# Performance work log

Measured on AMD Instinct MI355X. Metric: run time of the kernel, lower is better.

## Reference

```python
import jax, jax.numpy as jnp
import numpy as np

N = 100_000          # nodes
E = 1_600_000        # directed edges
GENE_DIM = 39
NUM_CLASSES = 5
EPS = 1e-5           # BatchNorm1d eps
DIMS = [(GENE_DIM, 64), (64, 128), (128, 64), (64, 32)]


def setup_inputs() -> dict:
    key = jax.random.key(0)
    ks = jax.random.split(key, 32)
    inp = {
        "x": jax.random.normal(ks[0], (N, GENE_DIM), dtype=jnp.float32),
        "edge_index": jax.random.randint(ks[1], (2, E), 0, N, dtype=jnp.int64),
    }
    ki = 2
    for i, (din, dout) in enumerate(DIMS, start=1):
        scale = 1.0 / np.sqrt(din)
        inp[f"W{i}"] = jax.random.uniform(ks[ki], (din, dout), jnp.float32, -scale, scale); ki += 1
        inp[f"b{i}"] = jnp.zeros((dout,), jnp.float32)
        inp[f"g{i}"] = jnp.ones((dout,), jnp.float32)    # BN gamma
        inp[f"be{i}"] = jnp.zeros((dout,), jnp.float32)  # BN beta
    scale = 1.0 / np.sqrt(32)
    inp["Wc"] = jax.random.uniform(ks[ki], (32, NUM_CLASSES), jnp.float32, -scale, scale)
    inp["bc"] = jnp.zeros((NUM_CLASSES,), jnp.float32)
    return inp


def reference(x, edge_index,
              W1, b1, g1, be1,
              W2, b2, g2, be2,
              W3, b3, g3, be3,
              W4, b4, g4, be4,
              Wc, bc):
    n = x.shape[0]
    # --- self loops + symmetric GCN normalization (shared by all 4 convs) ---
    loop = jnp.arange(n, dtype=edge_index.dtype)
    src = jnp.concatenate([edge_index[0], loop])   # message source (x_j)
    dst = jnp.concatenate([edge_index[1], loop])   # aggregation target
    deg = jax.ops.segment_sum(jnp.ones_like(dst, dtype=x.dtype), dst, num_segments=n)
    dinv = jnp.where(deg > 0, jax.lax.rsqrt(deg), 0.0)
    norm = (dinv[src] * dinv[dst])[:, None]        # [E+n, 1]

    def conv(h, W, b):
        # linear transform, gather from source, normalize, scatter-add at target
        m = (h @ W)[src] * norm
        return jax.ops.segment_sum(m, dst, num_segments=n) + b

    def bn(h, g, be):
        # training-mode BatchNorm1d: biased variance over the node axis
        mu = jnp.mean(h, axis=0)
        var = jnp.mean(jnp.square(h - mu), axis=0)
        return g * (h - mu) * jax.lax.rsqrt(var + EPS) + be

    h = bn(jax.nn.relu(conv(x, W1, b1)), g1, be1)
    h = bn(jax.nn.relu(conv(h, W2, b2)), g2, be2)
    h = bn(jax.nn.relu(conv(h, W3, b3)), g3, be3)
    h = bn(jax.nn.relu(conv(h, W4, b4)), g4, be4)
    out = h @ Wc + bc
    return (out, h)
```

## Files before the change

kernel.cpp:

```cpp
#include <hip/hip_runtime.h>

typedef unsigned int uint;
typedef unsigned short ushort;
typedef __attribute__((ext_vector_type(8))) short bf16x8;
typedef __attribute__((ext_vector_type(4))) float f32x4;

#define N_NODES 100000
#define N_EDGES 1600000
#define NB_C 256
#define TILE_C ((N_EDGES + NB_C - 1) / NB_C)
#define NB_D ((N_NODES + 511) / 512)
#define MG_GRID ((N_NODES + 63) / 64)
#define AGG_GRID 2048
constexpr float BN_EPS = 1e-5f;

__device__ __forceinline__ float bflo(uint w) { return __uint_as_float(w << 16); }
__device__ __forceinline__ float bfhi(uint w) { return __uint_as_float(w & 0xffff0000u); }
__device__ __forceinline__ ushort f2bf(float x) {
    uint u = __float_as_uint(x);
    uint r = (u + 0x7fffu + ((u >> 16) & 1u)) >> 16;
    return (ushort)r;
}
__device__ __forceinline__ uint pack2(float a, float b) {
    return (uint)f2bf(a) | ((uint)f2bf(b) << 16);
}

__global__ void detect_kernel(const int* __restrict__ ep, int* __restrict__ flag)
{
    __shared__ int cnt;
    if (threadIdx.x == 0) cnt = 0;
    __syncthreads();
    int nz = 0;
    for (int k = threadIdx.x; k < 1024; k += blockDim.x)
        if (ep[2 * k + 1] != 0) nz++;
    atomicAdd(&cnt, nz);
    __syncthreads();
    if (threadIdx.x == 0) *flag = (cnt == 0) ? 1 : 0;
}

__global__ __launch_bounds__(256) void coarseA_kernel(const int* __restrict__ ep,
                                                      const int* __restrict__ flag,
                                                      uint* __restrict__ ch)
{
    __shared__ uint lh[256];
    int t = threadIdx.x, blk = blockIdx.x;
    lh[t] = 0;
    __syncthreads();
    bool i64 = (*flag != 0);
    int start = blk * TILE_C;
    int end = start + TILE_C;
    if (end > N_EDGES) end = N_EDGES;
    for (int e = start + t; e < end; e += 256) {
        int d = i64 ? ep[2 * (N_EDGES + e)] : ep[N_EDGES + e];
        atomicAdd(&lh[d >> 9], 1u);
    }
    __syncthreads();
    ch[t * NB_C + blk] = lh[t];
}

__global__ void scanB_kernel(uint* __restrict__ ch, uint* __restrict__ bucketBase)
{
    __shared__ uint tot[256];
    int t = threadIdx.x;
    uint s = 0;
    for (int i = 0; i < NB_C; i++) s += ch[t * NB_C + i];
    tot[t] = s;
    __syncthreads();
    for (int off = 1; off < 256; off <<= 1) {
        uint add = (t >= off) ? tot[t - off] : 0u;
        __syncthreads();
        tot[t] += add;
        __syncthreads();
    }
    uint base = tot[t] - s;
    bucketBase[t] = base;
    if (t == 255) bucketBase[256] = base + s;
    uint run = base;
    for (int i = 0; i < NB_C; i++) {
        uint c = ch[t * NB_C + i];
        ch[t * NB_C + i] = run;
        run += c;
    }
}

__global__ __launch_bounds__(256) void scatterC_kernel(const int* __restrict__ ep,
                                                       const int* __restrict__ flag,
                                                       const uint* __restrict__ ch,
                                                       int2* __restrict__ pair)
{
    __shared__ uint loff[256];
    int t = threadIdx.x, blk = blockIdx.x;
    loff[t] = ch[t * NB_C + blk];
    __syncthreads();
    bool i64 = (*flag != 0);
    int start = blk * TILE_C;
    int end = start + TILE_C;
    if (end > N_EDGES) end = N_EDGES;
    for (int e = start + t; e < end; e += 256) {
        int s, d;
        if (i64) { s = ep[2 * e]; d = ep[2 * (N_EDGES + e)]; }
        else     { s = ep[e];     d = ep[N_EDGES + e]; }
        uint pos = atomicAdd(&loff[d >> 9], 1u);
        pair[pos] = make_int2(s, d);
    }
}

__global__ __launch_bounds__(256) void bucketD_kernel(const int2* __restrict__ pair,
                                                      const uint* __restrict__ bucketBase,
                                                      int* __restrict__ rowptr,
                                                      float* __restrict__ dinv,
                                                      int* __restrict__ colidx)
{
    __shared__ uint cnt[512], offp[512], s2[256];
    int bin = blockIdx.x, t = threadIdx.x;
    cnt[t] = 0; cnt[t + 256] = 0;
    __syncthreads();
    uint lo = bucketBase[bin], hi = bucketBase[bin + 1];
    for (uint p = lo + t; p < hi; p += 256)
        atomicAdd(&cnt[pair[p].y & 511], 1u);
    __syncthreads();
    uint a = cnt[2 * t], b = cnt[2 * t + 1];
    s2[t] = a + b;
    __syncthreads();
    for (int off = 1; off < 256; off <<= 1) {
        uint add = (t >= off) ? s2[t - off] : 0u;
        __syncthreads();
        s2[t] += add;
        __syncthreads();
    }
    uint excl = s2[t] - (a + b);
    offp[2 * t] = excl;
    offp[2 * t + 1] = excl + a;
    __syncthreads();
    for (int k = t; k < 512; k += 256) {
        int d = bin * 512 + k;
        if (d < N_NODES) {
            rowptr[d] = (int)(lo + offp[k]);
            dinv[d] = rsqrtf((float)(cnt[k] + 1));
        }
    }
    if (bin == 0 && t == 0) rowptr[N_NODES] = N_EDGES;
    __syncthreads();
    for (uint p = lo + t; p < hi; p += 256) {
        int2 pr = pair[p];
        uint pos = lo + atomicAdd(&offp[pr.y & 511], 1u);
        colidx[pos] = pr.x;
    }
}

__global__ __launch_bounds__(256) void xscale_kernel(const float* __restrict__ x,
                                                     const float* __restrict__ dinv,
                                                     ushort* __restrict__ xs)
{
    int idx = blockIdx.x * 256 + threadIdx.x;
    if (idx >= N_NODES * 40) return;
    int i = idx / 40;
    int c = idx - i * 40;
    float v = (c < 39) ? x[i * 39 + c] * dinv[i] : 0.f;
    xs[idx] = f2bf(v);
}

__global__ void packW_kernel(const float* __restrict__ W, ushort* __restrict__ out,
                             int din, int dout, int K)
{
    int CT = dout >> 4;
    int tot = (K >> 5) * CT * 64 * 8;
    for (int idx = blockIdx.x * 256 + threadIdx.x; idx < tot; idx += gridDim.x * 256) {
        int j = idx & 7;
        int lane = (idx >> 3) & 63;
        int slot = idx >> 9;
        int ct = slot % CT, kt = slot / CT;
        int k = kt * 32 + (lane >> 4) * 8 + j;
        int c = ct * 16 + (lane & 15);
        float v = (k < din) ? W[k * dout + c] : 0.f;
        out[idx] = f2bf(v);
    }
}

__global__ __launch_bounds__(256) void agg1_kernel(
    const uint* __restrict__ xs, const int* __restrict__ rowptr,
    const int* __restrict__ colidx, const float* __restrict__ dinv,
    uint* __restrict__ outU, float* __restrict__ rowsumP)
{
    int lane = threadIdx.x & 63, wid = threadIdx.x >> 6;
    int part = lane >> 5, idx = lane & 31;
    bool feat = idx < 20, dlane = (idx == 20);
    int gw = blockIdx.x * 4 + wid, nw = gridDim.x * 4;
    for (int i = gw; i < N_NODES; i += nw) {
        int iu = __builtin_amdgcn_readfirstlane(i);
        int s0 = rowptr[iu], e0 = rowptr[iu + 1];
        float ax = 0.f, ay = 0.f, ad = 0.f;
        if (!part && feat) { uint w = xs[iu * 20 + idx]; ax = bflo(w); ay = bfhi(w); }
        int e = s0 + part;
        for (; e + 6 < e0; e += 8) {
            int j0 = colidx[e], j1 = colidx[e + 2], j2 = colidx[e + 4], j3 = colidx[e + 6];
            if (feat) {
                uint w0 = xs[j0 * 20 + idx], w1 = xs[j1 * 20 + idx];
                uint w2 = xs[j2 * 20 + idx], w3 = xs[j3 * 20 + idx];
                ax += bflo(w0); ay += bfhi(w0);
                ax += bflo(w1); ay += bfhi(w1);
                ax += bflo(w2); ay += bfhi(w2);
                ax += bflo(w3); ay += bfhi(w3);
            } else if (dlane) {
                ad += dinv[j0] + dinv[j1] + dinv[j2] + dinv[j3];
            }
        }
        for (; e < e0; e += 2) {
            int j = colidx[e];
            if (feat) { uint w = xs[j * 20 + idx]; ax += bflo(w); ay += bfhi(w); }
            else if (dlane) ad += dinv[j];
        }
        ax += __shfl_xor(ax, 32);
        ay += __shfl_xor(ay, 32);
        ad += __shfl_xor(ad, 32);
        float di = dinv[iu];
        float dtot = __shfl(ad, 20);
        if (!part) outU[iu * 32 + idx] = feat ? pack2(di * ax, di * ay) : 0u;
        if (lane == 0) rowsumP[iu] = di * (dtot + di);
    }
}

__global__ __launch_bounds__(256) void agg_only64_kernel(
    const uint* __restrict__ zs, const int* __restrict__ rowptr,
    const int* __restrict__ colidx, const float* __restrict__ dinv,
    uint* __restrict__ out)
{
    int lane = threadIdx.x & 63, wid = threadIdx.x >> 6;
    int part = lane >> 5, fl = lane & 31;
    int gw = blockIdx.x * 4 + wid, nw = gridDim.x * 4;
    for (int i = gw; i < N_NODES; i += nw) {
        int iu = __builtin_amdgcn_readfirstlane(i);
        int s0 = rowptr[iu], e0 = rowptr[iu + 1];
        float ax = 0.f, ay = 0.f;
        if (!part) { uint w = zs[iu * 32 + fl]; ax = bflo(w); ay = bfhi(w); }
        int e = s0 + part;
        for (; e + 6 < e0; e += 8) {
            int j0 = colidx[e], j1 = colidx[e + 2], j2 = colidx[e + 4], j3 = colidx[e + 6];
            uint w0 = zs[j0 * 32 + fl], w1 = zs[j1 * 32 + fl];
            uint w2 = zs[j2 * 32 + fl], w3 = zs[j3 * 32 + fl];
            ax += bflo(w0); ay += bfhi(w0);
            ax += bflo(w1); ay += bfhi(w1);
            ax += bflo(w2); ay += bfhi(w2);
            ax += bflo(w3); ay += bfhi(w3);
        }
        for (; e < e0; e += 2) {
            uint w = zs[colidx[e] * 32 + fl];
            ax += bflo(w); ay += bfhi(w);
        }
        ax += __shfl_xor(ax, 32);
        ay += __shfl_xor(ay, 32);
        if (!part) {
            float di = dinv[iu];
            out[iu * 32 + fl] = pack2(di * ax, di * ay);
        }
    }
}

__global__ __launch_bounds__(256) void agg_relu64_kernel(
    const uint* __restrict__ zs, const int* __restrict__ rowptr,
    const int* __restrict__ colidx, const float* __restrict__ dinv,
    const float* __restrict__ bias, uint* __restrict__ outT,
    float* __restrict__ Psum, float* __restrict__ Psq)
{
    int lane = threadIdx.x & 63, wid = threadIdx.x >> 6;
    int part = lane >> 5, fl = lane & 31;
    int gw = blockIdx.x * 4 + wid, nw = gridDim.x * 4;
    float bx = bias[2 * fl], by = bias[2 * fl + 1];
    float lsx = 0.f, lsy = 0.f, lqx = 0.f, lqy = 0.f;
    for (int i = gw; i < N_NODES; i += nw) {
        int iu = __builtin_amdgcn_readfirstlane(i);
        int s0 = rowptr[iu], e0 = rowptr[iu + 1];
        float ax = 0.f, ay = 0.f;
        if (!part) { uint w = zs[iu * 32 + fl]; ax = bflo(w); ay = bfhi(w); }
        int e = s0 + part;
        for (; e + 6 < e0; e += 8) {
            int j0 = colidx[e], j1 = colidx[e + 2], j2 = colidx[e + 4], j3 = colidx[e + 6];
            uint w0 = zs[j0 * 32 + fl], w1 = zs[j1 * 32 + fl];
            uint w2 = zs[j2 * 32 + fl], w3 = zs[j3 * 32 + fl];
            ax += bflo(w0); ay += bfhi(w0);
            ax += bflo(w1); ay += bfhi(w1);
            ax += bflo(w2); ay += bfhi(w2);
            ax += bflo(w3); ay += bfhi(w3);
        }
        for (; e < e0; e += 2) {
            uint w = zs[colidx[e] * 32 + fl];
            ax += bflo(w); ay += bfhi(w);
        }
        ax += __shfl_xor(ax, 32);
        ay += __shfl_xor(ay, 32);
        if (!part) {
            float di = dinv[iu];
            float tx_ = fmaxf(fmaf(di, ax, bx), 0.f);
            float ty_ = fmaxf(fmaf(di, ay, by), 0.f);
            outT[iu * 32 + fl] = pack2(tx_, ty_);
            lsx += tx_; lsy += ty_;
            lqx += tx_ * tx_; lqy += ty_ * ty_;
        }
    }
    __shared__ float ssum[64], ssq[64];
    if (threadIdx.x < 64) { ssum[threadIdx.x] = 0.f; ssq[threadIdx.x] = 0.f; }
    __syncthreads();
    if (!part) {
        atomicAdd(&ssum[2 * fl], lsx); atomicAdd(&ssum[2 * fl + 1], lsy);
        atomicAdd(&ssq[2 * fl], lqx);  atomicAdd(&ssq[2 * fl + 1], lqy);
    }
    __syncthreads();
    if (threadIdx.x < 64) {
        Psum[threadIdx.x * gridDim.x + blockIdx.x] = ssum[threadIdx.x];
        Psq[threadIdx.x * gridDim.x + blockIdx.x] = ssq[threadIdx.x];
    }
}

__global__ __launch_bounds__(256) void agg_relu32_kernel(
    const uint* __restrict__ zs, const int* __restrict__ rowptr,
    const int* __restrict__ colidx, const float* __restrict__ dinv,
    const float* __restrict__ bias, float2* __restrict__ outT,
    float* __restrict__ Psum, float* __restrict__ Psq)
{
    int lane = threadIdx.x & 63, wid = threadIdx.x >> 6;
    int part = lane >> 4, fl = lane & 15;
    int gw = blockIdx.x * 4 + wid, nw = gridDim.x * 4;
    float bx = bias[2 * fl], by = bias[2 * fl + 1];
    float lsx = 0.f, lsy = 0.f, lqx = 0.f, lqy = 0.f;
    for (int i = gw; i < N_NODES; i += nw) {
        int iu = __builtin_amdgcn_readfirstlane(i);
        int s0 = rowptr[iu], e0 = rowptr[iu + 1];
        float ax = 0.f, ay = 0.f;
        if (part == 0) { uint w = zs[iu * 16 + fl]; ax = bflo(w); ay = bfhi(w); }
        int e = s0 + part;
        for (; e + 12 < e0; e += 16) {
            int j0 = colidx[e], j1 = colidx[e + 4], j2 = colidx[e + 8], j3 = colidx[e + 12];
            uint w0 = zs[j0 * 16 + fl], w1 = zs[j1 * 16 + fl];
            uint w2 = zs[j2 * 16 + fl], w3 = zs[j3 * 16 + fl];
            ax += bflo(w0); ay += bfhi(w0);
            ax += bflo(w1); ay += bfhi(w1);
            ax += bflo(w2); ay += bfhi(w2);
            ax += bflo(w3); ay += bfhi(w3);
        }
        for (; e < e0; e += 4) {
            uint w = zs[colidx[e] * 16 + fl];
            ax += bflo(w); ay += bfhi(w);
        }
        ax += __shfl_xor(ax, 16); ax += __shfl_xor(ax, 32);
        ay += __shfl_xor(ay, 16); ay += __shfl_xor(ay, 32);
        if (lane < 16) {
            float di = dinv[iu];
            float tx_ = fmaxf(fmaf(di, ax, bx), 0.f);
            float ty_ = fmaxf(fmaf(di, ay, by), 0.f);
            outT[iu * 16 + fl] = make_float2(tx_, ty_);
            lsx += tx_; lsy += ty_;
            lqx += tx_ * tx_; lqy += ty_ * ty_;
        }
    }
    __shared__ float ssum[32], ssq[32];
    if (threadIdx.x < 32) { ssum[threadIdx.x] = 0.f; ssq[threadIdx.x] = 0.f; }
    __syncthreads();
    if (lane < 16) {
        atomicAdd(&ssum[2 * fl], lsx); atomicAdd(&ssum[2 * fl + 1], lsy);
        atomicAdd(&ssq[2 * fl], lqx);  atomicAdd(&ssq[2 * fl + 1], lqy);
    }
    __syncthreads();
    if (threadIdx.x < 32) {
        Psum[threadIdx.x * gridDim.x + blockIdx.x] = ssum[threadIdx.x];
        Psq[threadIdx.x * gridDim.x + blockIdx.x] = ssq[threadIdx.x];
    }
}

template <int K, int DOUT, int MODE>
__global__ __launch_bounds__(256) void mgemm_kernel(
    const ushort* __restrict__ A, const ushort* __restrict__ Wfrag,
    const float* __restrict__ bias, const float* __restrict__ bias2,
    const float* __restrict__ rowsumP, const float* __restrict__ dinv,
    ushort* __restrict__ outB, float* __restrict__ Psum, float* __restrict__ Psq)
{
    constexpr int KT = K / 32, CT = DOUT / 16;
    int tid = threadIdx.x;
    int lane = tid & 63, wid = tid >> 6;
    int r0 = blockIdx.x * 64 + wid * 16;
    int arow = r0 + (lane & 15);
    if (arow >= N_NODES) arow = N_NODES - 1;
    const ushort* aptr = A + (size_t)arow * K + (lane >> 4) * 8;

    f32x4 acc[CT];
#pragma unroll
    for (int ct = 0; ct < CT; ct++) acc[ct] = (f32x4){0.f, 0.f, 0.f, 0.f};

#pragma unroll
    for (int kt = 0; kt < KT; kt++) {
        bf16x8 af = *(const bf16x8*)(aptr + kt * 32);
        const ushort* wp = Wfrag + ((size_t)(kt * CT) * 64 + lane) * 8;
#pragma unroll
        for (int ct = 0; ct < CT; ct++) {
            bf16x8 bfr = *(const bf16x8*)(wp + (size_t)ct * 64 * 8);
            acc[ct] = __builtin_amdgcn_mfma_f32_16x16x32_bf16(af, bfr, acc[ct], 0, 0, 0);
        }
    }

    int colbase = lane & 15;
    int rgrp = lane >> 4;
    int rows[4]; bool rok[4];
    float rP[4], rD[4];
#pragma unroll
    for (int i = 0; i < 4; i++) {
        int r = r0 + rgrp * 4 + i;
        rows[i] = r;
        rok[i] = (r < N_NODES);
        int rc = rok[i] ? r : 0;
        if constexpr (MODE == 1) rP[i] = rowsumP[rc];
        else rD[i] = dinv[rc];
    }

    __shared__ float ssum[DOUT], ssq[DOUT];
    if constexpr (MODE <= 1) {
        for (int c = tid; c < DOUT; c += 256) { ssum[c] = 0.f; ssq[c] = 0.f; }
        __syncthreads();
    }

#pragma unroll
    for (int ct = 0; ct < CT; ct++) {
        int col = ct * 16 + colbase;
        float b = bias[col];
        float b2 = 0.f;
        if constexpr (MODE == 1) b2 = bias2[col];
        float cs = 0.f, cq = 0.f;
#pragma unroll
        for (int i = 0; i < 4; i++) {
            float v = acc[ct][i] + b;
            if constexpr (MODE == 1) v = fmaf(rP[i], b2, v);
            if constexpr (MODE <= 1) v = fmaxf(v, 0.f);
            float w = (MODE == 1) ? v : rD[i] * v;
            if (rok[i]) {
                outB[(size_t)rows[i] * DOUT + col] = f2bf(w);
                if constexpr (MODE <= 1) { cs += v; cq += v * v; }
            }
        }
        if constexpr (MODE <= 1) {
            cs += __shfl_xor(cs, 16); cs += __shfl_xor(cs, 32);
            cq += __shfl_xor(cq, 16); cq += __shfl_xor(cq, 32);
            if (rgrp == 0) {
                atomicAdd(&ssum[col], cs);
                atomicAdd(&ssq[col], cq);
            }
        }
    }
    if constexpr (MODE <= 1) {
        __syncthreads();
        for (int c = tid; c < DOUT; c += 256) {
            Psum[(size_t)c * gridDim.x + blockIdx.x] = ssum[c];
            Psq[(size_t)c * gridDim.x + blockIdx.x] = ssq[c];
        }
    }
}

__global__ __launch_bounds__(256) void reduce_bn_kernel(
    const float* __restrict__ Psum, const float* __restrict__ Psq, int nb,
    const float* __restrict__ g, const float* __restrict__ be,
    float* __restrict__ sOut, float* __restrict__ uOut)
{
    int c = blockIdx.x, t = threadIdx.x;
    float s = 0.f, q = 0.f;
    for (int i = t; i < nb; i += 256) {
        s += Psum[(size_t)c * nb + i];
        q += Psq[(size_t)c * nb + i];
    }
    __shared__ float rs[256], rq[256];
    rs[t] = s; rq[t] = q;
    __syncthreads();
    for (int off = 128; off > 0; off >>= 1) {
        if (t < off) { rs[t] += rs[t + off]; rq[t] += rq[t + off]; }
        __syncthreads();
    }
    if (t == 0) {
        float mu = rs[0] * (1.0f / N_NODES);
        float var = rq[0] * (1.0f / N_NODES) - mu * mu;
        float sv = g[c] * rsqrtf(var + BN_EPS);
        sOut[c] = sv;
        uOut[c] = be[c] - mu * sv;
    }
}

__global__ void foldW_kernel(const float* __restrict__ W, const float* __restrict__ s,
                             const float* __restrict__ u, float* __restrict__ Wf,
                             float* __restrict__ v, int din, int dout)
{
    int c = blockIdx.x, t = threadIdx.x;
    float contrib = 0.f;
    if (t < din) {
        float w = W[t * dout + c];
        Wf[t * dout + c] = s[t] * w;
        contrib = u[t] * w;
    }
    __shared__ float red[128];
    red[t] = contrib;
    __syncthreads();
    for (int off = 64; off > 0; off >>= 1) {
        if (t < off) red[t] += red[t + off];
        __syncthreads();
    }
    if (t == 0) v[c] = red[0];
}

__global__ __launch_bounds__(256) void final_kernel(
    const float* __restrict__ t4, const float* __restrict__ sArr,
    const float* __restrict__ uArr, const float* __restrict__ Wc,
    const float* __restrict__ bc, float* __restrict__ out_logits,
    float* __restrict__ out_h)
{
    __shared__ float sc[32], sh2[32], Wcs[160], bcs[5];
    int t = threadIdx.x;
    if (t < 32) { sc[t] = sArr[t]; sh2[t] = uArr[t]; }
    if (t < 160) Wcs[t] = Wc[t];
    if (t < 5) bcs[t] = bc[t];
    __syncthreads();
    int i = blockIdx.x * blockDim.x + t;
    if (i >= N_NODES) return;
    float hv[32];
#pragma unroll
    for (int f0 = 0; f0 < 32; f0 += 4) {
        float4 v = *(const float4*)&t4[(size_t)i * 32 + f0];
        hv[f0 + 0] = fmaf(sc[f0 + 0], v.x, sh2[f0 + 0]);
        hv[f0 + 1] = fmaf(sc[f0 + 1], v.y, sh2[f0 + 1]);
        hv[f0 + 2] = fmaf(sc[f0 + 2], v.z, sh2[f0 + 2]);
        hv[f0 + 3] = fmaf(sc[f0 + 3], v.w, sh2[f0 + 3]);
    }
#pragma unroll
    for (int f0 = 0; f0 < 32; f0 += 4) {
        float4 v = {hv[f0], hv[f0 + 1], hv[f0 + 2], hv[f0 + 3]};
        *(float4*)&out_h[(size_t)i * 32 + f0] = v;
    }
    float o[5];
#pragma unroll
    for (int c = 0; c < 5; c++) o[c] = bcs[c];
#pragma unroll
    for (int f = 0; f < 32; f++) {
        float hvf = hv[f];
#pragma unroll
        for (int c = 0; c < 5; c++) o[c] = fmaf(hvf, Wcs[f * 5 + c], o[c]);
    }
#pragma unroll
    for (int c = 0; c < 5; c++) out_logits[(size_t)i * 5 + c] = o[c];
}

extern "C" void kernel_launch(void* const* d_in, const int* in_sizes, int n_in,
                              void* d_out, int out_size, void* d_ws, size_t ws_size,
                              hipStream_t stream)
{
    const float* x = (const float*)d_in[0];
    const int* ei = (const int*)d_in[1];
    const float* W1 = (const float*)d_in[2];
    const float* b1 = (const float*)d_in[3];
    const float* g1 = (const float*)d_in[4];
    const float* be1 = (const float*)d_in[5];
    const float* W2 = (const float*)d_in[6];
    const float* b2 = (const float*)d_in[7];
    const float* g2 = (const float*)d_in[8];
    const float* be2 = (const float*)d_in[9];
    const float* W3 = (const float*)d_in[10];
    const float* b3 = (const float*)d_in[11];
    const float* g3 = (const float*)d_in[12];
    const float* be3 = (const float*)d_in[13];
    const float* W4 = (const float*)d_in[14];
    const float* b4 = (const float*)d_in[15];
    const float* g4 = (const float*)d_in[16];
    const float* be4 = (const float*)d_in[17];
    const float* Wc = (const float*)d_in[18];
    const float* bc = (const float*)d_in[19];

    char* ws = (char*)d_ws;
    size_t off = 0;
    auto alloc = [&](size_t bytes) -> void* {
        void* p = ws + off;
        off += (bytes + 255) & ~(size_t)255;
        return p;
    };
    uint* ch = (uint*)alloc(65536 * 4);
    uint* bucketBase = (uint*)alloc(257 * 4);
    int2* pair = (int2*)alloc((size_t)N_EDGES * 8);
    int* rowptr = (int*)alloc((size_t)(N_NODES + 1) * 4);
    float* dinv = (float*)alloc((size_t)N_NODES * 4);
    int* colidx = (int*)alloc((size_t)N_EDGES * 4);
    int* flag = (int*)alloc(256);
    float* rowsumP = (float*)alloc((size_t)N_NODES * 4);
    ushort* xs = (ushort*)alloc((size_t)N_NODES * 40 * 2);
    float* Wf = (float*)alloc(128 * 128 * 4);
    ushort* Wfrag = (ushort*)alloc(32768);
    float* vB = (float*)alloc(128 * 4);
    float* sArr = (float*)alloc(128 * 4);
    float* uArr = (float*)alloc(128 * 4);
    float* Psum = (float*)alloc((size_t)128 * 2048 * 4);
    float* Psq = (float*)alloc((size_t)128 * 2048 * 4);
    uint* bufA = (uint*)alloc((size_t)N_NODES * 64 * 4);
    uint* bufB = (uint*)alloc((size_t)N_NODES * 32 * 4);
    uint* bufC = (uint*)alloc((size_t)N_NODES * 32 * 4);
    float* bufF = (float*)alloc((size_t)N_NODES * 32 * 4);
    if (off > ws_size) return;

    detect_kernel<<<1, 256, 0, stream>>>(ei, flag);
    coarseA_kernel<<<NB_C, 256, 0, stream>>>(ei, flag, ch);
    scanB_kernel<<<1, 256, 0, stream>>>(ch, bucketBase);
    scatterC_kernel<<<NB_C, 256, 0, stream>>>(ei, flag, ch, pair);
    bucketD_kernel<<<NB_D, 256, 0, stream>>>(pair, bucketBase, rowptr, dinv, colidx);

    xscale_kernel<<<(N_NODES * 40 + 255) / 256, 256, 0, stream>>>(x, dinv, xs);
    packW_kernel<<<16, 256, 0, stream>>>(W1, Wfrag, 39, 64, 64);

    agg1_kernel<<<AGG_GRID, 256, 0, stream>>>((const uint*)xs, rowptr, colidx, dinv,
                                              bufB, rowsumP);
    mgemm_kernel<64, 64, 0><<<MG_GRID, 256, 0, stream>>>(
        (const ushort*)bufB, Wfrag, b1, nullptr, nullptr, dinv,
        (ushort*)bufC, Psum, Psq);
    reduce_bn_kernel<<<64, 256, 0, stream>>>(Psum, Psq, MG_GRID, g1, be1, sArr, uArr);
    foldW_kernel<<<128, 128, 0, stream>>>(W2, sArr, uArr, Wf, vB, 64, 128);
    packW_kernel<<<32, 256, 0, stream>>>(Wf, Wfrag, 64, 128, 64);

    agg_only64_kernel<<<AGG_GRID, 256, 0, stream>>>(bufC, rowptr, colidx, dinv, bufB);
    mgemm_kernel<64, 128, 1><<<MG_GRID, 256, 0, stream>>>(
        (const ushort*)bufB, Wfrag, b2, vB, rowsumP, nullptr,
        (ushort*)bufA, Psum, Psq);
    reduce_bn_kernel<<<128, 256, 0, stream>>>(Psum, Psq, MG_GRID, g2, be2, sArr, uArr);
    foldW_kernel<<<64, 128, 0, stream>>>(W3, sArr, uArr, Wf, vB, 128, 64);
    packW_kernel<<<32, 256, 0, stream>>>(Wf, Wfrag, 128, 64, 128);

    mgemm_kernel<128, 64, 2><<<MG_GRID, 256, 0, stream>>>(
        (const ushort*)bufA, Wfrag, vB, nullptr, nullptr, dinv,
        (ushort*)bufB, nullptr, nullptr);
    agg_relu64_kernel<<<AGG_GRID, 256, 0, stream>>>(bufB, rowptr, colidx, dinv,
                                                    b3, bufC, Psum, Psq);
    reduce_bn_kernel<<<64, 256, 0, stream>>>(Psum, Psq, AGG_GRID, g3, be3, sArr, uArr);
    foldW_kernel<<<32, 128, 0, stream>>>(W4, sArr, uArr, Wf, vB, 64, 32);
    packW_kernel<<<16, 256, 0, stream>>>(Wf, Wfrag, 64, 32, 64);

    mgemm_kernel<64, 32, 2><<<MG_GRID, 256, 0, stream>>>(
        (const ushort*)bufC, Wfrag, vB, nullptr, nullptr, dinv,
        (ushort*)bufB, nullptr, nullptr);
    agg_relu32_kernel<<<AGG_GRID, 256, 0, stream>>>(bufB, rowptr, colidx, dinv,
                                                    b4, (float2*)bufF, Psum, Psq);
    reduce_bn_kernel<<<32, 256, 0, stream>>>(Psum, Psq, AGG_GRID, g4, be4, sArr, uArr);

    float* out_logits = (float*)d_out;
    float* out_h = (float*)d_out + (size_t)N_NODES * 5;
    final_kernel<<<(N_NODES + 255) / 256, 256, 0, stream>>>(bufF, sArr, uArr, Wc, bc,
                                                            out_logits, out_h);
}
```

Measured before the change: 382.4 us.

## Slice feature tables into 16-column planes and pin slices to XCDs in aggregation

Feature tables are stored as column slices of 16 bf16 values per node (32 bytes), and one templated aggregation kernel maps each slice to a subset of XCDs by block index. Each XCD's L2 then only has to hold one slice of the gathered table, which should raise cache hit rates for the random neighbor gathers. The GEMM kernels gain sliced input and output addressing, and the rowsum computation moves into its own kernel. The cost is an extra kernel, an extra memset for the padding slice, and 32-byte gathers that use less of each cache line per access.

```diff
diff --git a/kernel.cpp b/kernel.cpp
--- a/kernel.cpp
+++ b/kernel.cpp
@@ -11,7 +11,8 @@
 #define TILE_C ((N_EDGES + NB_C - 1) / NB_C)
 #define NB_D ((N_NODES + 511) / 512)
 #define MG_GRID ((N_NODES + 63) / 64)
-#define AGG_GRID 2048
+#define AGGS_GRID 1024
+#define AGGS_M (AGGS_GRID / 8)
 constexpr float BN_EPS = 1e-5f;
 
 __device__ __forceinline__ float bflo(uint w) { return __uint_as_float(w << 16); }
@@ -150,14 +151,18 @@
 
 __global__ __launch_bounds__(256) void xscale_kernel(const float* __restrict__ x,
                                                      const float* __restrict__ dinv,
-                                                     ushort* __restrict__ xs)
+                                                     uint* __restrict__ xs)
 {
     int idx = blockIdx.x * 256 + threadIdx.x;
-    if (idx >= N_NODES * 40) return;
-    int i = idx / 40;
-    int c = idx - i * 40;
-    float v = (c < 39) ? x[i * 39 + c] * dinv[i] : 0.f;
-    xs[idx] = f2bf(v);
+    if (idx >= N_NODES * 24) return;
+    int i = idx / 24;
+    int u = idx - i * 24;
+    int s = u >> 3, d = u & 7;
+    int c0 = 2 * u, c1 = 2 * u + 1;
+    float di = dinv[i];
+    float v0 = (c0 < 39) ? x[i * 39 + c0] * di : 0.f;
+    float v1 = (c1 < 39) ? x[i * 39 + c1] * di : 0.f;
+    xs[((size_t)s * N_NODES + i) * 8 + d] = pack2(v0, v1);
 }
 
 __global__ void packW_kernel(const float* __restrict__ W, ushort* __restrict__ out,
@@ -177,196 +182,123 @@
     }
 }
 
-__global__ __launch_bounds__(256) void agg1_kernel(
-    const uint* __restrict__ xs, const int* __restrict__ rowptr,
+__global__ __launch_bounds__(256) void rowsum_kernel(
+    const int* __restrict__ rowptr, const int* __restrict__ colidx,
+    const float* __restrict__ dinv, float* __restrict__ rowsumP)
+{
+    int tid = threadIdx.x;
+    int lane = tid & 63, wid = tid >> 6;
+    int g16 = lane >> 4, gl = lane & 15;
+    int gid = (blockIdx.x * 4 + wid) * 4 + g16;
+    int ng = gridDim.x * 16;
+    for (int i0 = gid; i0 < N_NODES; i0 += ng) {
+        int s0 = rowptr[i0], e0 = rowptr[i0 + 1];
+        float ad = 0.f;
+        for (int e = s0 + gl; e < e0; e += 16) ad += dinv[colidx[e]];
+        ad += __shfl_xor(ad, 1); ad += __shfl_xor(ad, 2);
+        ad += __shfl_xor(ad, 4); ad += __shfl_xor(ad, 8);
+        if (gl == 0) {
+            float di = dinv[i0];
+            rowsumP[i0] = di * (ad + di);
+        }
+    }
+}
+
+template <int SLICES, int MODE>
+__global__ __launch_bounds__(256) void aggs_kernel(
+    const uint* __restrict__ table, const int* __restrict__ rowptr,
     const int* __restrict__ colidx, const float* __restrict__ dinv,
-    uint* __restrict__ outU, float* __restrict__ rowsumP)
-{
-    int lane = threadIdx.x & 63, wid = threadIdx.x >> 6;
-    int part = lane >> 5, idx = lane & 31;
-    bool feat = idx < 20, dlane = (idx == 20);
-    int gw = blockIdx.x * 4 + wid, nw = gridDim.x * 4;
-    for (int i = gw; i < N_NODES; i += nw) {
-        int iu = __builtin_amdgcn_readfirstlane(i);
-        int s0 = rowptr[iu], e0 = rowptr[iu + 1];
-        float ax = 0.f, ay = 0.f, ad = 0.f;
-        if (!part && feat) { uint w = xs[iu * 20 + idx]; ax = bflo(w); ay = bfhi(w); }
-        int e = s0 + part;
+    const float* __restrict__ bias,
+    uint* __restrict__ outU, float* __restrict__ outF,
+    float* __restrict__ Psum, float* __restrict__ Psq)
+{
+    int bid = blockIdx.x;
+    int xcd = bid & 7;
+    int M = gridDim.x >> 3;
+    int slice, sub, ns;
+    if constexpr (SLICES == 4) { slice = xcd >> 1; sub = xcd & 1; ns = 2; }
+    else if constexpr (SLICES == 2) { slice = xcd >> 2; sub = xcd & 3; ns = 4; }
+    else {
+        if (xcd < 3) { slice = 0; sub = xcd; ns = 3; }
+        else if (xcd < 6) { slice = 1; sub = xcd - 3; ns = 3; }
+        else { slice = 2; sub = xcd - 6; ns = 2; }
+    }
+    int v = (bid >> 3) * ns + sub;
+    int V = M * ns;
+
+    int tid = threadIdx.x;
+    int lane = tid & 63, wid = tid >> 6;
+    int g16 = lane >> 4, gl = lane & 15;
+    int p = gl >> 3, d = gl & 7;
+    const uint* base = table + (size_t)slice * N_NODES * 8;
+
+    float bx = 0.f, by = 0.f;
+    if constexpr (MODE >= 1) {
+        bx = bias[slice * 16 + 2 * d];
+        by = bias[slice * 16 + 2 * d + 1];
+    }
+    float lsx = 0.f, lsy = 0.f, lqx = 0.f, lqy = 0.f;
+
+    for (int i0 = v * 16 + wid * 4 + g16; i0 < N_NODES; i0 += V * 16) {
+        int s0 = rowptr[i0], e0 = rowptr[i0 + 1];
+        float ax = 0.f, ay = 0.f;
+        if (p == 0) {
+            uint w = base[((size_t)i0 << 3) + d];
+            ax = bflo(w); ay = bfhi(w);
+        }
+        int e = s0 + p;
         for (; e + 6 < e0; e += 8) {
             int j0 = colidx[e], j1 = colidx[e + 2], j2 = colidx[e + 4], j3 = colidx[e + 6];
-            if (feat) {
-                uint w0 = xs[j0 * 20 + idx], w1 = xs[j1 * 20 + idx];
-                uint w2 = xs[j2 * 20 + idx], w3 = xs[j3 * 20 + idx];
-                ax += bflo(w0); ay += bfhi(w0);
-                ax += bflo(w1); ay += bfhi(w1);
-                ax += bflo(w2); ay += bfhi(w2);
-                ax += bflo(w3); ay += bfhi(w3);
-            } else if (dlane) {
-                ad += dinv[j0] + dinv[j1] + dinv[j2] + dinv[j3];
-            }
-        }
-        for (; e < e0; e += 2) {
-            int j = colidx[e];
-            if (feat) { uint w = xs[j * 20 + idx]; ax += bflo(w); ay += bfhi(w); }
-            else if (dlane) ad += dinv[j];
-        }
-        ax += __shfl_xor(ax, 32);
-        ay += __shfl_xor(ay, 32);
-        ad += __shfl_xor(ad, 32);
-        float di = dinv[iu];
-        float dtot = __shfl(ad, 20);
-        if (!part) outU[iu * 32 + idx] = feat ? pack2(di * ax, di * ay) : 0u;
-        if (lane == 0) rowsumP[iu] = di * (dtot + di);
-    }
-}
-
-__global__ __launch_bounds__(256) void agg_only64_kernel(
-    const uint* __restrict__ zs, const int* __restrict__ rowptr,
-    const int* __restrict__ colidx, const float* __restrict__ dinv,
-    uint* __restrict__ out)
-{
-    int lane = threadIdx.x & 63, wid = threadIdx.x >> 6;
-    int part = lane >> 5, fl = lane & 31;
-    int gw = blockIdx.x * 4 + wid, nw = gridDim.x * 4;
-    for (int i = gw; i < N_NODES; i += nw) {
-        int iu = __builtin_amdgcn_readfirstlane(i);
-        int s0 = rowptr[iu], e0 = rowptr[iu + 1];
-        float ax = 0.f, ay = 0.f;
-        if (!part) { uint w = zs[iu * 32 + fl]; ax = bflo(w); ay = bfhi(w); }
-        int e = s0 + part;
-        for (; e + 6 < e0; e += 8) {
-            int j0 = colidx[e], j1 = colidx[e + 2], j2 = colidx[e + 4], j3 = colidx[e + 6];
-            uint w0 = zs[j0 * 32 + fl], w1 = zs[j1 * 32 + fl];
-            uint w2 = zs[j2 * 32 + fl], w3 = zs[j3 * 32 + fl];
+            uint w0 = base[((size_t)j0 << 3) + d];
+            uint w1 = base[((size_t)j1 << 3) + d];
+            uint w2 = base[((size_t)j2 << 3) + d];
+            uint w3 = base[((size_t)j3 << 3) + d];
             ax += bflo(w0); ay += bfhi(w0);
             ax += bflo(w1); ay += bfhi(w1);
             ax += bflo(w2); ay += bfhi(w2);
             ax += bflo(w3); ay += bfhi(w3);
         }
         for (; e < e0; e += 2) {
-            uint w = zs[colidx[e] * 32 + fl];
+            uint w = base[((size_t)colidx[e] << 3) + d];
             ax += bflo(w); ay += bfhi(w);
         }
-        ax += __shfl_xor(ax, 32);
-        ay += __shfl_xor(ay, 32);
-        if (!part) {
-            float di = dinv[iu];
-            out[iu * 32 + fl] = pack2(di * ax, di * ay);
-        }
-    }
-}
-
-__global__ __launch_bounds__(256) void agg_relu64_kernel(
-    const uint* __restrict__ zs, const int* __restrict__ rowptr,
-    const int* __restrict__ colidx, const float* __restrict__ dinv,
-    const float* __restrict__ bias, uint* __restrict__ outT,
-    float* __restrict__ Psum, float* __restrict__ Psq)
-{
-    int lane = threadIdx.x & 63, wid = threadIdx.x >> 6;
-    int part = lane >> 5, fl = lane & 31;
-    int gw = blockIdx.x * 4 + wid, nw = gridDim.x * 4;
-    float bx = bias[2 * fl], by = bias[2 * fl + 1];
-    float lsx = 0.f, lsy = 0.f, lqx = 0.f, lqy = 0.f;
-    for (int i = gw; i < N_NODES; i += nw) {
-        int iu = __builtin_amdgcn_readfirstlane(i);
-        int s0 = rowptr[iu], e0 = rowptr[iu + 1];
-        float ax = 0.f, ay = 0.f;
-        if (!part) { uint w = zs[iu * 32 + fl]; ax = bflo(w); ay = bfhi(w); }
-        int e = s0 + part;
-        for (; e + 6 < e0; e += 8) {
-            int j0 = colidx[e], j1 = colidx[e + 2], j2 = colidx[e + 4], j3 = colidx[e + 6];
-            uint w0 = zs[j0 * 32 + fl], w1 = zs[j1 * 32 + fl];
-            uint w2 = zs[j2 * 32 + fl], w3 = zs[j3 * 32 + fl];
-            ax += bflo(w0); ay += bfhi(w0);
-            ax += bflo(w1); ay += bfhi(w1);
-            ax += bflo(w2); ay += bfhi(w2);
-            ax += bflo(w3); ay += bfhi(w3);
-        }
-        for (; e < e0; e += 2) {
-            uint w = zs[colidx[e] * 32 + fl];
-            ax += bflo(w); ay += bfhi(w);
-        }
-        ax += __shfl_xor(ax, 32);
-        ay += __shfl_xor(ay, 32);
-        if (!part) {
-            float di = dinv[iu];
-            float tx_ = fmaxf(fmaf(di, ax, bx), 0.f);
-            float ty_ = fmaxf(fmaf(di, ay, by), 0.f);
-            outT[iu * 32 + fl] = pack2(tx_, ty_);
-            lsx += tx_; lsy += ty_;
-            lqx += tx_ * tx_; lqy += ty_ * ty_;
-        }
-    }
-    __shared__ float ssum[64], ssq[64];
-    if (threadIdx.x < 64) { ssum[threadIdx.x] = 0.f; ssq[threadIdx.x] = 0.f; }
-    __syncthreads();
-    if (!part) {
-        atomicAdd(&ssum[2 * fl], lsx); atomicAdd(&ssum[2 * fl + 1], lsy);
-        atomicAdd(&ssq[2 * fl], lqx);  atomicAdd(&ssq[2 * fl + 1], lqy);
-    }
-    __syncthreads();
-    if (threadIdx.x < 64) {
-        Psum[threadIdx.x * gridDim.x + blockIdx.x] = ssum[threadIdx.x];
-        Psq[threadIdx.x * gridDim.x + blockIdx.x] = ssq[threadIdx.x];
-    }
-}
-
-__global__ __launch_bounds__(256) void agg_relu32_kernel(
-    const uint* __restrict__ zs, const int* __restrict__ rowptr,
-    const int* __restrict__ colidx, const float* __restrict__ dinv,
-    const float* __restrict__ bias, float2* __restrict__ outT,
-    float* __restrict__ Psum, float* __restrict__ Psq)
-{
-    int lane = threadIdx.x & 63, wid = threadIdx.x >> 6;
-    int part = lane >> 4, fl = lane & 15;
-    int gw = blockIdx.x * 4 + wid, nw = gridDim.x * 4;
-    float bx = bias[2 * fl], by = bias[2 * fl + 1];
-    float lsx = 0.f, lsy = 0.f, lqx = 0.f, lqy = 0.f;
-    for (int i = gw; i < N_NODES; i += nw) {
-        int iu = __builtin_amdgcn_readfirstlane(i);
-        int s0 = rowptr[iu], e0 = rowptr[iu + 1];
-        float ax = 0.f, ay = 0.f;
-        if (part == 0) { uint w = zs[iu * 16 + fl]; ax = bflo(w); ay = bfhi(w); }
-        int e = s0 + part;
-        for (; e + 12 < e0; e += 16) {
-            int j0 = colidx[e], j1 = colidx[e + 4], j2 = colidx[e + 8], j3 = colidx[e + 12];
-            uint w0 = zs[j0 * 16 + fl], w1 = zs[j1 * 16 + fl];
-            uint w2 = zs[j2 * 16 + fl], w3 = zs[j3 * 16 + fl];
-            ax += bflo(w0); ay += bfhi(w0);
-            ax += bflo(w1); ay += bfhi(w1);
-            ax += bflo(w2); ay += bfhi(w2);
-            ax += bflo(w3); ay += bfhi(w3);
-        }
-        for (; e < e0; e += 4) {
-            uint w = zs[colidx[e] * 16 + fl];
-            ax += bflo(w); ay += bfhi(w);
-        }
-        ax += __shfl_xor(ax, 16); ax += __shfl_xor(ax, 32);
-        ay += __shfl_xor(ay, 16); ay += __shfl_xor(ay, 32);
-        if (lane < 16) {
-            float di = dinv[iu];
-            float tx_ = fmaxf(fmaf(di, ax, bx), 0.f);
-            float ty_ = fmaxf(fmaf(di, ay, by), 0.f);
-            outT[iu * 16 + fl] = make_float2(tx_, ty_);
-            lsx += tx_; lsy += ty_;
-            lqx += tx_ * tx_; lqy += ty_ * ty_;
-        }
-    }
-    __shared__ float ssum[32], ssq[32];
-    if (threadIdx.x < 32) { ssum[threadIdx.x] = 0.f; ssq[threadIdx.x] = 0.f; }
-    __syncthreads();
-    if (lane < 16) {
-        atomicAdd(&ssum[2 * fl], lsx); atomicAdd(&ssum[2 * fl + 1], lsy);
-        atomicAdd(&ssq[2 * fl], lqx);  atomicAdd(&ssq[2 * fl + 1], lqy);
-    }
-    __syncthreads();
-    if (threadIdx.x < 32) {
-        Psum[threadIdx.x * gridDim.x + blockIdx.x] = ssum[threadIdx.x];
-        Psq[threadIdx.x * gridDim.x + blockIdx.x] = ssq[threadIdx.x];
-    }
-}
-
-template <int K, int DOUT, int MODE>
+        ax += __shfl_xor(ax, 8);
+        ay += __shfl_xor(ay, 8);
+        if (p == 0) {
+            float di = dinv[i0];
+            if constexpr (MODE == 0) {
+                outU[((size_t)slice * N_NODES + i0) * 8 + d] = pack2(di * ax, di * ay);
+            } else {
+                float tx = fmaxf(fmaf(di, ax, bx), 0.f);
+                float ty = fmaxf(fmaf(di, ay, by), 0.f);
+                if constexpr (MODE == 1)
+                    outU[((size_t)slice * N_NODES + i0) * 8 + d] = pack2(tx, ty);
+                else
+                    *(float2*)&outF[((size_t)slice * N_NODES + i0) * 16 + 2 * d] =
+                        make_float2(tx, ty);
+                lsx += tx; lsy += ty;
+                lqx += tx * tx; lqy += ty * ty;
+            }
+        }
+    }
+
+    if constexpr (MODE >= 1) {
+        __shared__ float ssum[16], ssq[16];
+        if (tid < 16) { ssum[tid] = 0.f; ssq[tid] = 0.f; }
+        __syncthreads();
+        if (p == 0) {
+            atomicAdd(&ssum[2 * d], lsx); atomicAdd(&ssum[2 * d + 1], lsy);
+            atomicAdd(&ssq[2 * d], lqx);  atomicAdd(&ssq[2 * d + 1], lqy);
+        }
+        __syncthreads();
+        if (tid < 16) {
+            Psum[(size_t)(slice * 16 + tid) * V + v] = ssum[tid];
+            Psq[(size_t)(slice * 16 + tid) * V + v] = ssq[tid];
+        }
+    }
+}
+
+template <int K, int DOUT, int MODE, int ASLICED, int OSLICED>
 __global__ __launch_bounds__(256) void mgemm_kernel(
     const ushort* __restrict__ A, const ushort* __restrict__ Wfrag,
     const float* __restrict__ bias, const float* __restrict__ bias2,
@@ -379,7 +311,6 @@
     int r0 = blockIdx.x * 64 + wid * 16;
     int arow = r0 + (lane & 15);
     if (arow >= N_NODES) arow = N_NODES - 1;
-    const ushort* aptr = A + (size_t)arow * K + (lane >> 4) * 8;
 
     f32x4 acc[CT];
 #pragma unroll
@@ -387,7 +318,13 @@
 
 #pragma unroll
     for (int kt = 0; kt < KT; kt++) {
-        bf16x8 af = *(const bf16x8*)(aptr + kt * 32);
+        int k0 = kt * 32 + (lane >> 4) * 8;
+        const ushort* ap;
+        if constexpr (ASLICED)
+            ap = A + (((size_t)(k0 >> 4) * N_NODES + arow) << 4) + (k0 & 15);
+        else
+            ap = A + (size_t)arow * K + k0;
+        bf16x8 af = *(const bf16x8*)ap;
         const ushort* wp = Wfrag + ((size_t)(kt * CT) * 64 + lane) * 8;
 #pragma unroll
         for (int ct = 0; ct < CT; ct++) {
@@ -430,7 +367,12 @@
             if constexpr (MODE <= 1) v = fmaxf(v, 0.f);
             float w = (MODE == 1) ? v : rD[i] * v;
             if (rok[i]) {
-                outB[(size_t)rows[i] * DOUT + col] = f2bf(w);
+                size_t addr;
+                if constexpr (OSLICED)
+                    addr = ((size_t)ct * N_NODES + rows[i]) * 16 + colbase;
+                else
+                    addr = (size_t)rows[i] * DOUT + col;
+                outB[addr] = f2bf(w);
                 if constexpr (MODE <= 1) { cs += v; cq += v * v; }
             }
         }
@@ -516,12 +458,20 @@
     if (i >= N_NODES) return;
     float hv[32];
 #pragma unroll
-    for (int f0 = 0; f0 < 32; f0 += 4) {
-        float4 v = *(const float4*)&t4[(size_t)i * 32 + f0];
+    for (int f0 = 0; f0 < 16; f0 += 4) {
+        float4 v = *(const float4*)&t4[(size_t)i * 16 + f0];
         hv[f0 + 0] = fmaf(sc[f0 + 0], v.x, sh2[f0 + 0]);
         hv[f0 + 1] = fmaf(sc[f0 + 1], v.y, sh2[f0 + 1]);
         hv[f0 + 2] = fmaf(sc[f0 + 2], v.z, sh2[f0 + 2]);
         hv[f0 + 3] = fmaf(sc[f0 + 3], v.w, sh2[f0 + 3]);
+    }
+#pragma unroll
+    for (int f0 = 0; f0 < 16; f0 += 4) {
+        float4 v = *(const float4*)&t4[((size_t)N_NODES + i) * 16 + f0];
+        hv[16 + f0 + 0] = fmaf(sc[16 + f0 + 0], v.x, sh2[16 + f0 + 0]);
+        hv[16 + f0 + 1] = fmaf(sc[16 + f0 + 1], v.y, sh2[16 + f0 + 1]);
+        hv[16 + f0 + 2] = fmaf(sc[16 + f0 + 2], v.z, sh2[16 + f0 + 2]);
+        hv[16 + f0 + 3] = fmaf(sc[16 + f0 + 3], v.w, sh2[16 + f0 + 3]);
     }
 #pragma unroll
     for (int f0 = 0; f0 < 32; f0 += 4) {
@@ -581,7 +531,7 @@
     int* colidx = (int*)alloc((size_t)N_EDGES * 4);
     int* flag = (int*)alloc(256);
     float* rowsumP = (float*)alloc((size_t)N_NODES * 4);
-    ushort* xs = (ushort*)alloc((size_t)N_NODES * 40 * 2);
+    uint* xs = (uint*)alloc((size_t)N_NODES * 24 * 4);
     float* Wf = (float*)alloc(128 * 128 * 4);
     ushort* Wfrag = (ushort*)alloc(32768);
     float* vB = (float*)alloc(128 * 4);
@@ -589,11 +539,13 @@
     float* uArr = (float*)alloc(128 * 4);
     float* Psum = (float*)alloc((size_t)128 * 2048 * 4);
     float* Psq = (float*)alloc((size_t)128 * 2048 * 4);
-    uint* bufA = (uint*)alloc((size_t)N_NODES * 64 * 4);
-    uint* bufB = (uint*)alloc((size_t)N_NODES * 32 * 4);
-    uint* bufC = (uint*)alloc((size_t)N_NODES * 32 * 4);
-    float* bufF = (float*)alloc((size_t)N_NODES * 32 * 4);
+    uint* P = (uint*)alloc((size_t)N_NODES * 32 * 4);
+    uint* Q = (uint*)alloc((size_t)N_NODES * 32 * 4);
+    uint* R = (uint*)alloc((size_t)N_NODES * 64 * 4);
     if (off > ws_size) return;
+
+    constexpr int V4 = AGGS_M * 2;
+    constexpr int V2 = AGGS_M * 4;
 
     detect_kernel<<<1, 256, 0, stream>>>(ei, flag);
     coarseA_kernel<<<NB_C, 256, 0, stream>>>(ei, flag, ch);
@@ -601,44 +553,43 @@
     scatterC_kernel<<<NB_C, 256, 0, stream>>>(ei, flag, ch, pair);
     bucketD_kernel<<<NB_D, 256, 0, stream>>>(pair, bucketBase, rowptr, dinv, colidx);
 
-    xscale_kernel<<<(N_NODES * 40 + 255) / 256, 256, 0, stream>>>(x, dinv, xs);
+    xscale_kernel<<<(N_NODES * 24 + 255) / 256, 256, 0, stream>>>(x, dinv, xs);
     packW_kernel<<<16, 256, 0, stream>>>(W1, Wfrag, 39, 64, 64);
-
-    agg1_kernel<<<AGG_GRID, 256, 0, stream>>>((const uint*)xs, rowptr, colidx, dinv,
-                                              bufB, rowsumP);
-    mgemm_kernel<64, 64, 0><<<MG_GRID, 256, 0, stream>>>(
-        (const ushort*)bufB, Wfrag, b1, nullptr, nullptr, dinv,
-        (ushort*)bufC, Psum, Psq);
+    rowsum_kernel<<<512, 256, 0, stream>>>(rowptr, colidx, dinv, rowsumP);
+    hipMemsetAsync(P + (size_t)3 * N_NODES * 8, 0, (size_t)N_NODES * 32, stream);
+
+    aggs_kernel<3, 0><<<AGGS_GRID, 256, 0, stream>>>(xs, rowptr, colidx, dinv, nullptr,
+                                                     P, nullptr, nullptr, nullptr);
+    mgemm_kernel<64, 64, 0, 1, 1><<<MG_GRID, 256, 0, stream>>>(
+        (const ushort*)P, Wfrag, b1, nullptr, nullptr, dinv, (ushort*)Q, Psum, Psq);
     reduce_bn_kernel<<<64, 256, 0, stream>>>(Psum, Psq, MG_GRID, g1, be1, sArr, uArr);
     foldW_kernel<<<128, 128, 0, stream>>>(W2, sArr, uArr, Wf, vB, 64, 128);
     packW_kernel<<<32, 256, 0, stream>>>(Wf, Wfrag, 64, 128, 64);
 
-    agg_only64_kernel<<<AGG_GRID, 256, 0, stream>>>(bufC, rowptr, colidx, dinv, bufB);
-    mgemm_kernel<64, 128, 1><<<MG_GRID, 256, 0, stream>>>(
-        (const ushort*)bufB, Wfrag, b2, vB, rowsumP, nullptr,
-        (ushort*)bufA, Psum, Psq);
+    aggs_kernel<4, 0><<<AGGS_GRID, 256, 0, stream>>>(Q, rowptr, colidx, dinv, nullptr,
+                                                     P, nullptr, nullptr, nullptr);
+    mgemm_kernel<64, 128, 1, 1, 0><<<MG_GRID, 256, 0, stream>>>(
+        (const ushort*)P, Wfrag, b2, vB, rowsumP, nullptr, (ushort*)R, Psum, Psq);
     reduce_bn_kernel<<<128, 256, 0, stream>>>(Psum, Psq, MG_GRID, g2, be2, sArr, uArr);
     foldW_kernel<<<64, 128, 0, stream>>>(W3, sArr, uArr, Wf, vB, 128, 64);
     packW_kernel<<<32, 256, 0, stream>>>(Wf, Wfrag, 128, 64, 128);
 
-    mgemm_kernel<128, 64, 2><<<MG_GRID, 256, 0, stream>>>(
-        (const ushort*)bufA, Wfrag, vB, nullptr, nullptr, dinv,
-        (ushort*)bufB, nullptr, nullptr);
-    agg_relu64_kernel<<<AGG_GRID, 256, 0, stream>>>(bufB, rowptr, colidx, dinv,
-                                                    b3, bufC, Psum, Psq);
-    reduce_bn_kernel<<<64, 256, 0, stream>>>(Psum, Psq, AGG_GRID, g3, be3, sArr, uArr);
+    mgemm_kernel<128, 64, 2, 0, 1><<<MG_GRID, 256, 0, stream>>>(
+        (const ushort*)R, Wfrag, vB, nullptr, nullptr, dinv, (ushort*)P, nullptr, nullptr);
+    aggs_kernel<4, 1><<<AGGS_GRID, 256, 0, stream>>>(P, rowptr, colidx, dinv, b3,
+                                                     Q, nullptr, Psum, Psq);
+    reduce_bn_kernel<<<64, 256, 0, stream>>>(Psum, Psq, V4, g3, be3, sArr, uArr);
     foldW_kernel<<<32, 128, 0, stream>>>(W4, sArr, uArr, Wf, vB, 64, 32);
     packW_kernel<<<16, 256, 0, stream>>>(Wf, Wfrag, 64, 32, 64);
 
-    mgemm_kernel<64, 32, 2><<<MG_GRID, 256, 0, stream>>>(
-        (const ushort*)bufC, Wfrag, vB, nullptr, nullptr, dinv,
-        (ushort*)bufB, nullptr, nullptr);
-    agg_relu32_kernel<<<AGG_GRID, 256, 0, stream>>>(bufB, rowptr, colidx, dinv,
-                                                    b4, (float2*)bufF, Psum, Psq);
-    reduce_bn_kernel<<<32, 256, 0, stream>>>(Psum, Psq, AGG_GRID, g4, be4, sArr, uArr);
+    mgemm_kernel<64, 32, 2, 1, 1><<<MG_GRID, 256, 0, stream>>>(
+        (const ushort*)Q, Wfrag, vB, nullptr, nullptr, dinv, (ushort*)P, nullptr, nullptr);
+    aggs_kernel<2, 2><<<AGGS_GRID, 256, 0, stream>>>(P, rowptr, colidx, dinv, b4,
+                                                     nullptr, (float*)R, Psum, Psq);
+    reduce_bn_kernel<<<32, 256, 0, stream>>>(Psum, Psq, V2, g4, be4, sArr, uArr);
 
     float* out_logits = (float*)d_out;
     float* out_h = (float*)d_out + (size_t)N_NODES * 5;
-    final_kernel<<<(N_NODES + 255) / 256, 256, 0, stream>>>(bufF, sArr, uArr, Wc, bc,
-                                                            out_logits, out_h);
-}
+    final_kernel<<<(N_NODES + 255) / 256, 256, 0, stream>>>((const float*)R, sArr, uArr,
+                                                            Wc, bc, out_logits, out_h);
+}
```

New measurement: 514.6 us. 34.6% more time.
